# Kernel tuning notes

Measured on AMD Instinct MI355X. Metric: run time of the kernel, lower is better.

## Reference

```python
import jax, jax.numpy as jnp
import numpy as np

BLOCK, HALO, HEADS = 8, 4, 4


def setup_inputs() -> dict:
    key = jax.random.key(0)
    ks = jax.random.split(key, 9)
    B, C, H, W = 8, 256, 64, 64
    inner = C  # heads * dim_head = 4 * 64
    d = inner // HEADS
    R = BLOCK + 2 * HALO  # 16
    s = 0.02
    return {
        "x": jax.random.normal(ks[0], (B, C, H, W), jnp.float32),
        "wq": jax.random.normal(ks[1], (inner, C), jnp.float32) * s,
        "wkv": jax.random.normal(ks[2], (2 * inner, C), jnp.float32) * s,
        "wo": jax.random.normal(ks[3], (C, inner), jnp.float32) * s,
        "bo": jax.random.normal(ks[4], (C,), jnp.float32) * s,
        "rel_h": jax.random.normal(ks[5], (2 * R - 1, d), jnp.float32) * (d ** -0.5),
        "rel_w": jax.random.normal(ks[6], (2 * R - 1, d), jnp.float32) * (d ** -0.5),
        "w_conv": jax.random.normal(ks[7], (4 * C, C), jnp.float32) * s,
        "b_conv": jax.random.normal(ks[8], (4 * C,), jnp.float32) * s,
    }


def reference(x, wq, wkv, wo, bo, rel_h, rel_w, w_conv, b_conv):
    B, C, H, W = x.shape
    bs, halo, heads = BLOCK, HALO, HEADS
    R = bs + 2 * halo
    inner = wq.shape[0]
    d = inner // heads
    nh, nw = H // bs, W // bs
    Nb = B * nh * nw

    # ---- HaloAttention ----
    # block queries: (B, C, nh, bs, nw, bs) -> (Nb, bs*bs, C)
    q_in = x.reshape(B, C, nh, bs, nw, bs).transpose(0, 2, 4, 3, 5, 1).reshape(Nb, bs * bs, C)
    # haloed K/V windows via overlapping gather (== F.unfold(kernel=R, stride=bs, pad=halo))
    xp = jnp.pad(x, ((0, 0), (0, 0), (halo, halo), (halo, halo)))
    ridx = (jnp.arange(nh) * bs)[:, None] + jnp.arange(R)[None]  # (nh, R)
    cidx = (jnp.arange(nw) * bs)[:, None] + jnp.arange(R)[None]  # (nw, R)
    win = xp[:, :, ridx][:, :, :, :, cidx]                       # (B, C, nh, R, nw, R)
    kv_in = win.transpose(0, 2, 4, 3, 5, 1).reshape(Nb, R * R, C)

    q = (q_in @ wq.T).reshape(Nb, bs * bs, heads, d).transpose(0, 2, 1, 3) * (d ** -0.5)
    kv = kv_in @ wkv.T
    k, v = jnp.split(kv, 2, axis=-1)
    k = k.reshape(Nb, R * R, heads, d).transpose(0, 2, 1, 3)
    v = v.reshape(Nb, R * R, heads, d).transpose(0, 2, 1, 3)

    sim = jnp.einsum('bhid,bhjd->bhij', q, k)  # (Nb, heads, bs*bs, R*R)

    # relative position logits (computed from the scaled q, as in the torch code)
    q5 = q.reshape(Nb, heads, bs, bs, d)
    rel_idx = jnp.arange(R)[None, :] - jnp.arange(bs)[:, None] + (R - 1)  # (bs, R)
    lw = jnp.einsum('bhxyd,yjd->bhxyj', q5, rel_w[rel_idx])  # over key col j
    lh = jnp.einsum('bhxyd,xid->bhxyi', q5, rel_h[rel_idx])  # over key row i
    sim = sim.reshape(Nb, heads, bs, bs, R, R) + lw[..., None, :] + lh[..., None]
    sim = sim.reshape(Nb, heads, bs * bs, R * R)

    # mask out padded halo positions
    m = jnp.pad(jnp.ones((H, W), bool), ((halo, halo), (halo, halo)))
    mwin = m[ridx][:, :, cidx].transpose(0, 2, 1, 3).reshape(nh * nw, R * R)
    mask = jnp.broadcast_to(mwin[None], (B, nh * nw, R * R)).reshape(Nb, 1, 1, R * R)
    sim = jnp.where(mask, sim, -jnp.finfo(sim.dtype).max)

    attn = jax.nn.softmax(sim, axis=-1)
    out = jnp.einsum('bhij,bhjd->bhid', attn, v)
    out = out.transpose(0, 2, 1, 3).reshape(Nb, bs * bs, inner)
    out = out @ wo.T + bo  # (Nb, bs*bs, C)
    y = out.reshape(B, nh, nw, bs, bs, C).transpose(0, 5, 1, 3, 2, 4).reshape(B, C, H, W)

    # ---- Conv2d(dim, 4*dim, 1) + PixelShuffle(2) ----
    y = jnp.einsum('bchw,oc->bohw', y, w_conv) + b_conv[None, :, None, None]
    Cn = y.shape[1] // 4
    y = y.reshape(B, Cn, 2, 2, H, W).transpose(0, 1, 4, 2, 5, 3).reshape(B, Cn, 2 * H, 2 * W)
    return y
```

## Files before the change

kernel.cpp:

```cpp
#include <hip/hip_runtime.h>

typedef unsigned short u16;
typedef unsigned int u32;
typedef __attribute__((ext_vector_type(8))) short short8;
typedef __attribute__((ext_vector_type(4))) float f32x4;

__device__ __forceinline__ float bf2f(u16 u){ union { u32 i; float f; } x; x.i = ((u32)u)<<16; return x.f; }
__device__ __forceinline__ u16 f2bf(float f){ union { float f; u32 i; } x; x.f = f; u32 r = x.i + 0x7fffu + ((x.i>>16)&1u); return (u16)(r>>16); }

#define MFMA16(a,b,c) __builtin_amdgcn_mfma_f32_16x16x32_bf16((a),(b),(c),0,0,0)

__device__ __forceinline__ uint4 ld8(const void* p, size_t off, int f32) {
  if (f32) {
    const float* fp = (const float*)p + off;
    float4 a = *(const float4*)fp;
    float4 b = *(const float4*)(fp + 4);
    uint4 o;
    o.x = (u32)f2bf(a.x) | ((u32)f2bf(a.y)<<16);
    o.y = (u32)f2bf(a.z) | ((u32)f2bf(a.w)<<16);
    o.z = (u32)f2bf(b.x) | ((u32)f2bf(b.y)<<16);
    o.w = (u32)f2bf(b.z) | ((u32)f2bf(b.w)<<16);
    return o;
  }
  return *(const uint4*)((const u16*)p + off);
}
__device__ __forceinline__ uint2 ld4(const void* p, size_t off, int f32) {
  if (f32) {
    const float* fp = (const float*)p + off;
    float4 a = *(const float4*)fp;
    uint2 o;
    o.x = (u32)f2bf(a.x) | ((u32)f2bf(a.y)<<16);
    o.y = (u32)f2bf(a.z) | ((u32)f2bf(a.w)<<16);
    return o;
  }
  return *(const uint2*)((const u16*)p + off);
}
__device__ __forceinline__ float ldsc(const void* p, size_t off, int f32) {
  if (f32) return ((const float*)p)[off];
  return bf2f(((const u16*)p)[off]);
}

__global__ __launch_bounds__(256) void k_detect(const u32* __restrict__ x, int* __restrict__ flag)
{
  __shared__ int cnt;
  if (threadIdx.x == 0) cnt = 0;
  __syncthreads();
  int c = 0;
  #pragma unroll
  for (int i = 0; i < 32; ++i) {
    u32 w = x[threadIdx.x*32 + i];
    u32 e = (w >> 7) & 0xFFu;
    c += (e == 0u || (e >= 96u && e <= 143u)) ? 1 : 0;
  }
  atomicAdd(&cnt, c);
  __syncthreads();
  if (threadIdx.x == 0) *flag = (cnt < 4915) ? 1 : 0;
}

__global__ __launch_bounds__(256) void k_transpose(const void* __restrict__ x, u16* __restrict__ xt,
                                                   const int* __restrict__ flagp)
{
  __shared__ int sflag;
  __shared__ __align__(16) u16 tile[64][68];
  if (threadIdx.x == 0) sflag = *flagp;
  __syncthreads();
  const int f32 = sflag;
  const int p0 = blockIdx.x*64, c0 = blockIdx.y*64, b = blockIdx.z;
  const int t = threadIdx.x;
  const size_t xbo = ((size_t)(b*256 + c0))*4096 + p0;
  #pragma unroll
  for (int pass=0; pass<4; ++pass) {
    int cl = pass*16 + (t>>4);
    int pl = (t&15)*4;
    uint2 v = ld4(x, xbo + (size_t)cl*4096 + pl, f32);
    *(uint2*)&tile[cl][pl] = v;
  }
  __syncthreads();
  u16* xtb = xt + ((size_t)b*4096 + p0)*256 + c0;
  #pragma unroll
  for (int pass=0; pass<4; ++pass) {
    int pl = pass*16 + (t>>4);
    int cl = (t&15)*4;
    unsigned int lo = (unsigned int)tile[cl][pl]   | ((unsigned int)tile[cl+1][pl]<<16);
    unsigned int hi = (unsigned int)tile[cl+2][pl] | ((unsigned int)tile[cl+3][pl]<<16);
    uint2 o; o.x = lo; o.y = hi;
    *(uint2*)(xtb + (size_t)pl*256 + cl) = o;
  }
}

__global__ __launch_bounds__(256) void k_gemm_bt(
  const u16* __restrict__ A, const void* __restrict__ Bt, const void* __restrict__ bias,
  void* __restrict__ C, int M, int N, int K, float scale, int shuffle,
  const int* __restrict__ flagp)
{
  __shared__ int sflag;
  __shared__ __align__(16) u16 Als[128*32];
  __shared__ __align__(16) u16 Bls[128*32];
  if (threadIdx.x == 0) sflag = *flagp;
  __syncthreads();
  const int f32 = sflag;
  const int m0 = blockIdx.x*128, n0 = blockIdx.y*128;
  const int t = threadIdx.x, lane = t & 63, wv = t >> 6;
  const int wm = (wv & 1)*64, wn = (wv >> 1)*64;
  const int lm = lane & 15, lq = lane >> 4;
  f32x4 acc[4][4] = {};
  for (int k0 = 0; k0 < K; k0 += 32) {
    #pragma unroll
    for (int i = 0; i < 2; ++i) {
      int u = t + i*256;
      int row = u >> 2, ch = (u & 3)*8;
      *(uint4*)&Als[row*32 + ch] = *(const uint4*)(A + (size_t)(m0+row)*K + k0 + ch);
      *(uint4*)&Bls[row*32 + ch] = ld8(Bt, (size_t)(n0+row)*K + k0 + ch, f32);
    }
    __syncthreads();
    short8 af[4], bf[4];
    #pragma unroll
    for (int i=0;i<4;++i) af[i] = *(const short8*)&Als[(wm + i*16 + lm)*32 + lq*8];
    #pragma unroll
    for (int i=0;i<4;++i) bf[i] = *(const short8*)&Bls[(wn + i*16 + lm)*32 + lq*8];
    #pragma unroll
    for (int mt=0;mt<4;++mt)
      #pragma unroll
      for (int nt=0;nt<4;++nt)
        acc[mt][nt] = MFMA16(af[mt], bf[nt], acc[mt][nt]);
    __syncthreads();
  }
  #pragma unroll
  for (int nt=0;nt<4;++nt) {
    int col = n0 + wn + nt*16 + lm;
    float bv = bias ? ldsc(bias, col, f32) : 0.0f;
    #pragma unroll
    for (int mt=0;mt<4;++mt) {
      #pragma unroll
      for (int r=0;r<4;++r) {
        int row = m0 + wm + mt*16 + lq*4 + r;
        float v = acc[mt][nt][r]*scale + bv;
        if (!shuffle) {
          ((u16*)C)[(size_t)row*N + col] = f2bf(v);
        } else {
          int b = row >> 12, hw = row & 4095;
          int hh = hw >> 6, ww = hw & 63;
          int cn = col >> 2, rr = (col >> 1) & 1, ss = col & 1;
          size_t idx = ((((size_t)(b*256 + cn))*128 + hh*2 + rr) << 7) + (size_t)(ww*2 + ss);
          if (f32) ((float*)C)[idx] = v;
          else     ((u16*)C)[idx]   = f2bf(v);
        }
      }
    }
  }
}

#define MASKVAL (-30000.0f)
__global__ __launch_bounds__(256) void k_halo_attn(
  const u16* __restrict__ qo, const u16* __restrict__ kv,
  const void* __restrict__ relh, const void* __restrict__ relw,
  u16* __restrict__ aout, const int* __restrict__ flagp)
{
  __shared__ int sflag;
  __shared__ __align__(16) u16 Qs[64*72];
  __shared__ __align__(16) u16 KP[128*72];
  __shared__ __align__(16) u16 Vt[64*136];
  __shared__ __align__(16) u16 Gw[64*32];
  __shared__ __align__(16) u16 Gh[64*32];
  if (threadIdx.x == 0) sflag = *flagp;
  __syncthreads();
  const int f32 = sflag;

  const int blk = blockIdx.x, head = blockIdx.y;
  const int bb = blk >> 6, by = (blk >> 3) & 7, bx = blk & 7;
  const int h0 = by*8, w0 = bx*8;
  const int t = threadIdx.x, lane = t & 63, wv = t >> 6;
  const int lm = lane & 15, lq = lane >> 4;
  const size_t pixbase = (size_t)bb * 4096;
  const float LOG2E = 1.4426950408889634f;

  #pragma unroll
  for (int i=0;i<2;++i) {
    int u = t + i*256;
    int row = u >> 3, ch = (u & 7)*8;
    int qx = row >> 3, qy = row & 7;
    size_t p = pixbase + (size_t)(h0+qx)*64 + (w0+qy);
    *(uint4*)&Qs[row*72 + ch] = *(const uint4*)(qo + p*256 + head*64 + ch);
  }
  {
    u16* RW = KP; u16* RH = KP + 2048;
    if (t < 248) {
      *(uint4*)&RW[t*8] = ld8(relw, (size_t)t*8, f32);
      *(uint4*)&RH[t*8] = ld8(relh, (size_t)t*8, f32);
    } else {
      uint4 z; z.x=z.y=z.z=z.w=0;
      int o = 1984 + (t-248)*8;
      *(uint4*)&RW[o] = z;
      *(uint4*)&RH[o] = z;
    }
  }
  __syncthreads();
  {
    const u16* RW = KP; const u16* RH = KP + 2048;
    f32x4 agw[2] = {}, agh[2] = {};
    #pragma unroll
    for (int ks=0;ks<2;++ks) {
      short8 aq = *(const short8*)&Qs[(wv*16 + lm)*72 + ks*32 + lq*8];
      #pragma unroll
      for (int nt=0;nt<2;++nt) {
        short8 bw = *(const short8*)&RW[(nt*16 + lm)*64 + ks*32 + lq*8];
        short8 bh = *(const short8*)&RH[(nt*16 + lm)*64 + ks*32 + lq*8];
        agw[nt] = MFMA16(aq, bw, agw[nt]);
        agh[nt] = MFMA16(aq, bh, agh[nt]);
      }
    }
    #pragma unroll
    for (int nt=0;nt<2;++nt)
      #pragma unroll
      for (int r=0;r<4;++r) {
        int m = wv*16 + lq*4 + r, c = nt*16 + lm;
        Gw[m*32 + c] = f2bf(agw[nt][r]);
        Gh[m*32 + c] = f2bf(agh[nt][r]);
      }
  }
  __syncthreads();

  float m_run[4], l_run[4];
  #pragma unroll
  for (int r=0;r<4;++r){ m_run[r] = MASKVAL; l_run[r] = 0.0f; }
  f32x4 acc_o[4] = {};

  for (int tile=0; tile<2; ++tile) {
    #pragma unroll
    for (int i=0;i<4;++i) {
      int u = t + i*256;
      int kl = u >> 3, ch = (u & 7)*8;
      int ki = tile*8 + (kl >> 4), kj = kl & 15;
      int hk = h0 - 4 + ki, wk = w0 - 4 + kj;
      uint4 v; v.x=v.y=v.z=v.w=0;
      if ((unsigned)hk < 64u && (unsigned)wk < 64u) {
        size_t p = pixbase + (size_t)hk*64 + wk;
        v = *(const uint4*)(kv + p*512 + head*64 + ch);
      }
      *(uint4*)&KP[kl*72 + ch] = v;
    }
    {
      int kl = t & 127, db = (t >> 7)*32;
      int ki = tile*8 + (kl >> 4), kj = kl & 15;
      int hk = h0 - 4 + ki, wk = w0 - 4 + kj;
      bool ok = ((unsigned)hk < 64u) && ((unsigned)wk < 64u);
      size_t p = pixbase + (size_t)hk*64 + wk;
      const u16* vp = kv + p*512 + 256 + head*64 + db;
      #pragma unroll
      for (int c=0;c<4;++c) {
        union { uint4 v; u16 s[8]; } uu;
        uu.v.x=uu.v.y=uu.v.z=uu.v.w=0;
        if (ok) uu.v = *(const uint4*)(vp + c*8);
        #pragma unroll
        for (int jj=0;jj<8;++jj) Vt[(db + c*8 + jj)*136 + kl] = uu.s[jj];
      }
    }
    __syncthreads();
    f32x4 as[8] = {};
    #pragma unroll
    for (int ks=0;ks<2;++ks) {
      short8 aq = *(const short8*)&Qs[(wv*16 + lm)*72 + ks*32 + lq*8];
      #pragma unroll
      for (int nt=0;nt<8;++nt) {
        short8 bk = *(const short8*)&KP[(nt*16 + lm)*72 + ks*32 + lq*8];
        as[nt] = MFMA16(aq, bk, as[nt]);
      }
    }
    __syncthreads();
    #pragma unroll
    for (int r=0;r<4;++r) {
      int m = wv*16 + lq*4 + r;
      int qx = m >> 3, qy = m & 7;
      float vals[8]; float rowmax = MASKVAL;
      #pragma unroll
      for (int nt=0;nt<8;++nt) {
        int ki = tile*8 + nt;
        int hk = h0 - 4 + ki, wk = w0 - 4 + lm;
        float v = as[nt][r]
                + bf2f(Gw[m*32 + (lm - qy + 15)])
                + bf2f(Gh[m*32 + (ki - qx + 15)]);
        if (!((unsigned)hk < 64u && (unsigned)wk < 64u)) v = MASKVAL;
        vals[nt] = v;
        rowmax = fmaxf(rowmax, v);
      }
      #pragma unroll
      for (int s=1;s<16;s<<=1) rowmax = fmaxf(rowmax, __shfl_xor(rowmax, s, 64));
      float mnew = fmaxf(m_run[r], rowmax);
      float alpha = exp2f((m_run[r] - mnew)*LOG2E);
      float rs = 0.0f;
      #pragma unroll
      for (int nt=0;nt<8;++nt) {
        float e = exp2f((vals[nt] - mnew)*LOG2E);
        rs += e;
        KP[m*136 + nt*16 + lm] = f2bf(e);
      }
      #pragma unroll
      for (int s=1;s<16;s<<=1) rs += __shfl_xor(rs, s, 64);
      l_run[r] = l_run[r]*alpha + rs;
      m_run[r] = mnew;
      #pragma unroll
      for (int nt=0;nt<4;++nt) acc_o[nt][r] *= alpha;
    }
    __syncthreads();
    #pragma unroll
    for (int ks=0;ks<4;++ks) {
      short8 ap = *(const short8*)&KP[(wv*16 + lm)*136 + ks*32 + lq*8];
      #pragma unroll
      for (int nt=0;nt<4;++nt) {
        short8 bv = *(const short8*)&Vt[(nt*16 + lm)*136 + ks*32 + lq*8];
        acc_o[nt] = MFMA16(ap, bv, acc_o[nt]);
      }
    }
    __syncthreads();
  }
  #pragma unroll
  for (int nt=0;nt<4;++nt)
    #pragma unroll
    for (int r=0;r<4;++r) {
      int m = wv*16 + lq*4 + r;
      int qx = m >> 3, qy = m & 7;
      size_t p = pixbase + (size_t)(h0+qx)*64 + (w0+qy);
      aout[p*256 + head*64 + nt*16 + lm] = f2bf(acc_o[nt][r]/l_run[r]);
    }
}

extern "C" void kernel_launch(void* const* d_in, const int* in_sizes, int n_in,
                              void* d_out, int out_size, void* d_ws, size_t ws_size,
                              hipStream_t stream)
{
  const void* x     = d_in[0];
  const void* wq    = d_in[1];
  const void* wkv   = d_in[2];
  const void* wo    = d_in[3];
  const void* bo    = d_in[4];
  const void* relh  = d_in[5];
  const void* relw  = d_in[6];
  const void* wconv = d_in[7];
  const void* bconv = d_in[8];

  int* flag = (int*)d_ws;
  u16* y2   = (u16*)((char*)d_ws + 4096);
  u16* base = (u16*)d_out;
  u16* kvb  = base;
  u16* qo   = base + 16777216;
  u16* xt   = base + 25165824;
  u16* aout = qo;

  k_detect<<<1, 256, 0, stream>>>((const u32*)x, flag);
  k_transpose<<<dim3(64,4,8), 256, 0, stream>>>(x, xt, flag);
  k_gemm_bt<<<dim3(256,2), 256, 0, stream>>>(xt, wq,  nullptr, qo,  32768, 256, 256, 0.125f, 0, flag);
  k_gemm_bt<<<dim3(256,4), 256, 0, stream>>>(xt, wkv, nullptr, kvb, 32768, 512, 256, 1.0f,   0, flag);
  k_halo_attn<<<dim3(512,4), 256, 0, stream>>>(qo, kvb, relh, relw, aout, flag);
  k_gemm_bt<<<dim3(256,2), 256, 0, stream>>>(aout, wo, bo, y2, 32768, 256, 256, 1.0f, 0, flag);
  k_gemm_bt<<<dim3(256,8), 256, 0, stream>>>(y2, wconv, bconv, d_out, 32768, 1024, 256, 1.0f, 1, flag);
}
```

Measured before the change: 426.1 us.

## Pad GEMM LDS tiles and stage epilogue through shared memory for coalesced stores

The GEMM's LDS row stride goes from 32 to 40 elements to cut bank conflicts on the MFMA fragment loads. The epilogue no longer does scattered per-element stores. It stages output tiles in shared memory, for both the plain layout and the pixel-shuffle layout, then writes contiguous 16-byte vectors to global memory. This adds extra barriers and LDS traffic in the epilogue, and the shuffle path assumes each 128-row block covers two full image rows.

```diff
diff --git a/kernel.cpp b/kernel.cpp
--- a/kernel.cpp
+++ b/kernel.cpp
@@ -94,8 +94,9 @@
   const int* __restrict__ flagp)
 {
   __shared__ int sflag;
-  __shared__ __align__(16) u16 Als[128*32];
-  __shared__ __align__(16) u16 Bls[128*32];
+  __shared__ __align__(16) char smem[20608];
+  u16* Als = (u16*)smem;
+  u16* Bls = (u16*)(smem + 10240);
   if (threadIdx.x == 0) sflag = *flagp;
   __syncthreads();
   const int f32 = sflag;
@@ -109,15 +110,15 @@
     for (int i = 0; i < 2; ++i) {
       int u = t + i*256;
       int row = u >> 2, ch = (u & 3)*8;
-      *(uint4*)&Als[row*32 + ch] = *(const uint4*)(A + (size_t)(m0+row)*K + k0 + ch);
-      *(uint4*)&Bls[row*32 + ch] = ld8(Bt, (size_t)(n0+row)*K + k0 + ch, f32);
+      *(uint4*)&Als[row*40 + ch] = *(const uint4*)(A + (size_t)(m0+row)*K + k0 + ch);
+      *(uint4*)&Bls[row*40 + ch] = ld8(Bt, (size_t)(n0+row)*K + k0 + ch, f32);
     }
     __syncthreads();
     short8 af[4], bf[4];
     #pragma unroll
-    for (int i=0;i<4;++i) af[i] = *(const short8*)&Als[(wm + i*16 + lm)*32 + lq*8];
-    #pragma unroll
-    for (int i=0;i<4;++i) bf[i] = *(const short8*)&Bls[(wn + i*16 + lm)*32 + lq*8];
+    for (int i=0;i<4;++i) af[i] = *(const short8*)&Als[(wm + i*16 + lm)*40 + lq*8];
+    #pragma unroll
+    for (int i=0;i<4;++i) bf[i] = *(const short8*)&Bls[(wn + i*16 + lm)*40 + lq*8];
     #pragma unroll
     for (int mt=0;mt<4;++mt)
       #pragma unroll
@@ -125,25 +126,81 @@
         acc[mt][nt] = MFMA16(af[mt], bf[nt], acc[mt][nt]);
     __syncthreads();
   }
-  #pragma unroll
-  for (int nt=0;nt<4;++nt) {
-    int col = n0 + wn + nt*16 + lm;
-    float bv = bias ? ldsc(bias, col, f32) : 0.0f;
-    #pragma unroll
-    for (int mt=0;mt<4;++mt) {
-      #pragma unroll
-      for (int r=0;r<4;++r) {
-        int row = m0 + wm + mt*16 + lq*4 + r;
-        float v = acc[mt][nt][r]*scale + bv;
-        if (!shuffle) {
-          ((u16*)C)[(size_t)row*N + col] = f2bf(v);
+
+  if (!shuffle) {
+    u16* eh = (u16*)smem;
+    #pragma unroll
+    for (int c=0;c<2;++c) {
+      __syncthreads();
+      if ((wv>>1) == c) {
+        #pragma unroll
+        for (int nt=0;nt<4;++nt) {
+          int col = n0 + c*64 + nt*16 + lm;
+          float bv = bias ? ldsc(bias, col, f32) : 0.0f;
+          #pragma unroll
+          for (int mt=0;mt<4;++mt)
+            #pragma unroll
+            for (int r=0;r<4;++r) {
+              int row = wm + mt*16 + lq*4 + r;
+              eh[row*72 + nt*16 + lm] = f2bf(acc[mt][nt][r]*scale + bv);
+            }
+        }
+      }
+      __syncthreads();
+      {
+        int row = t >> 1, off = (t & 1)*32;
+        const uint4* s = (const uint4*)&eh[row*72 + off];
+        uint4 v0 = s[0], v1 = s[1], v2 = s[2], v3 = s[3];
+        uint4* dp = (uint4*)((u16*)C + (size_t)(m0+row)*N + n0 + c*64 + off);
+        dp[0]=v0; dp[1]=v1; dp[2]=v2; dp[3]=v3;
+      }
+    }
+  } else {
+    float* ef = (float*)smem;
+    const int b = m0 >> 12;
+    const int hh0 = (m0 & 4095) >> 6;
+    #pragma unroll
+    for (int c=0;c<4;++c) {
+      __syncthreads();
+      if ((wv>>1) == (c>>1)) {
+        #pragma unroll
+        for (int nt2=0;nt2<2;++nt2) {
+          int nt = (c&1)*2 + nt2;
+          int col = n0 + wn + nt*16 + lm;
+          float bv = bias ? ldsc(bias, col, f32) : 0.0f;
+          int col_rel = nt2*16 + lm;
+          int cn_rel = col_rel >> 2, rr = (col_rel >> 1) & 1, ss = col_rel & 1;
+          #pragma unroll
+          for (int mt=0;mt<4;++mt)
+            #pragma unroll
+            for (int r=0;r<4;++r) {
+              int row = wm + mt*16 + lq*4 + r;
+              int orow = cn_rel*4 + (row>>6)*2 + rr;
+              int ow   = (row & 63)*2 + ss;
+              ef[orow*136 + ow] = acc[mt][nt][r]*scale + bv;
+            }
+        }
+      }
+      __syncthreads();
+      {
+        int orow = t >> 3, seg = t & 7;
+        int cn_rel = orow >> 2, oh_rel = orow & 3;
+        int cn = ((n0 + c*32) >> 2) + cn_rel;
+        size_t obase = (((size_t)(b*256 + cn))*128 + hh0*2 + oh_rel)*128 + seg*16;
+        const float4* s = (const float4*)&ef[orow*136 + seg*16];
+        float4 v0 = s[0], v1 = s[1], v2 = s[2], v3 = s[3];
+        if (f32) {
+          float4* dp = (float4*)((float*)C + obase);
+          dp[0]=v0; dp[1]=v1; dp[2]=v2; dp[3]=v3;
         } else {
-          int b = row >> 12, hw = row & 4095;
-          int hh = hw >> 6, ww = hw & 63;
-          int cn = col >> 2, rr = (col >> 1) & 1, ss = col & 1;
-          size_t idx = ((((size_t)(b*256 + cn))*128 + hh*2 + rr) << 7) + (size_t)(ww*2 + ss);
-          if (f32) ((float*)C)[idx] = v;
-          else     ((u16*)C)[idx]   = f2bf(v);
+          float vv[16];
+          *(float4*)&vv[0]=v0; *(float4*)&vv[4]=v1; *(float4*)&vv[8]=v2; *(float4*)&vv[12]=v3;
+          u32 pw[8];
+          #pragma unroll
+          for (int j=0;j<8;++j) pw[j] = (u32)f2bf(vv[2*j]) | ((u32)f2bf(vv[2*j+1])<<16);
+          u16* dp = (u16*)C + obase;
+          *(uint4*)dp       = *(uint4*)&pw[0];
+          *(uint4*)(dp + 8) = *(uint4*)&pw[4];
         }
       }
     }
```

Measured after the change: 406.4 us. 4.6% less time.
